# Kernel tuning notes

Measured on AMD Instinct MI355X. Metric: run time of the kernel, lower is better.

Reference implementation:

```python
import jax, jax.numpy as jnp
import numpy as np

B, N, T, L, H = 8, 128, 256, 32, 128


def setup_inputs() -> dict:
    key = jax.random.key(0)
    k0, k1, k2, k3, k4, k5 = jax.random.split(key, 6)
    x = jax.random.uniform(k0, (B, N, T), dtype=jnp.float32)
    s = 1.0 / np.sqrt(H)  # pytorch LSTM/Linear default init scale
    W_ih = jax.random.uniform(k1, (N, 4 * H, L), minval=-s, maxval=s, dtype=jnp.float32)
    b_ih = jax.random.uniform(k2, (N, 4 * H), minval=-s, maxval=s, dtype=jnp.float32)
    b_hh = jax.random.uniform(k3, (N, 4 * H), minval=-s, maxval=s, dtype=jnp.float32)
    W_fc = jax.random.uniform(k4, (N, N, H), minval=-s, maxval=s, dtype=jnp.float32)  # [node_i, out_j, H]
    b_fc = jax.random.uniform(k5, (N, N), minval=-s, maxval=s, dtype=jnp.float32)  # [node_i, out_j]
    return {"x": x, "W_ih": W_ih, "b_ih": b_ih, "b_hh": b_hh, "W_fc": W_fc, "b_fc": b_fc}


def reference(x, W_ih, b_ih, b_hh, W_fc, b_fc):
    # x: [B, N, T]
    Bn, Nn, Tn = x.shape
    Ln = W_ih.shape[-1]
    Hh = W_fc.shape[-1]
    Ttau = Tn - Ln  # number of prediction steps (t = L .. T-1)

    # Sliding windows x[:, i, tau:tau+L] for tau = 0..Ttau-1  -> [B, N, Ttau, L]
    idx = jnp.arange(Ttau)[:, None] + jnp.arange(Ln)[None, :]  # [Ttau, L]
    xw = x[:, :, idx]

    # Single-step LSTM with zero initial state: W_hh term vanishes.
    gates = jnp.einsum('bntl,ngl->bntg', xw, W_ih) + (b_ih + b_hh)[None, :, None, :]
    gi, gf, gg, go = jnp.split(gates, 4, axis=-1)  # pytorch order: i, f, g, o
    c = jax.nn.sigmoid(gi) * jnp.tanh(gg)          # f*c0 = 0
    h = jax.nn.sigmoid(go) * jnp.tanh(c)           # [B, N, Ttau, H]

    # Per-node fc (grouped GEMM): contributions[b, tau, j, i]
    contrib = jnp.einsum('bnth,njh->btjn', h, W_fc) + b_fc.T[None, None, :, :]

    # G[b, j, i] = mean_tau contrib[b, tau, j, i] / x[b, i, L + tau]
    denom = jnp.transpose(x[:, :, Ln:], (0, 2, 1))[:, :, None, :]  # [B, Ttau, 1, N_i]
    G = jnp.mean(contrib / denom, axis=1)                          # [B, N, N]

    X_hat = jnp.sum(contrib, axis=2) + 1e-6  # [B, Ttau, N]
    return G, X_hat
```

## Files before the change

kernel.cpp:

```cpp
#include <hip/hip_runtime.h>
#include <math.h>

#define B_  8
#define N_  128
#define T_  256
#define L_  32
#define H_  128
#define TT_ 224

typedef float f4    __attribute__((ext_vector_type(4)));
typedef float f32x4 __attribute__((ext_vector_type(4)));
typedef short bf16x8 __attribute__((ext_vector_type(8)));

__device__ __forceinline__ unsigned pk2bf(float a, float b) {
    unsigned ua = __float_as_uint(a), ub = __float_as_uint(b);
    ua = (ua + 0x7FFFu + ((ua >> 16) & 1u)) >> 16;
    ub = (ub + 0x7FFFu + ((ub >> 16) & 1u)) >> 16;
    return ua | (ub << 16);
}

__global__ __launch_bounds__(256)
void k_pre(const float* __restrict__ W_ih, const float* __restrict__ W_fc,
           const float* __restrict__ b_ih, const float* __restrict__ b_hh,
           const float* __restrict__ b_fc,
           unsigned short* __restrict__ W3sw, float* __restrict__ wsum,
           float* __restrict__ bsum, float* __restrict__ bia_g) {
    const int n   = blockIdx.x;
    const int pid = blockIdx.y;
    const int tid = threadIdx.x;
    if (pid < 6) {
        const int idx  = pid * 256 + tid;
        const int fg   = idx >> 6;
        const int lane = idx & 63;
        const int col  = lane & 15, quad = lane >> 4;
        const int g    = fg % 3, ht = fg / 3;
        const int r    = g * 128 + ht * 16 + col;
        const int sr   = r + (r >= 128 ? 128 : 0);
        const f4* src = (const f4*)(W_ih + (size_t)n * 512 * L_ + sr * L_ + quad * 8);
        f4 v0 = src[0], v1 = src[1];
        uint4 out;
        out.x = pk2bf(v0.x, v0.y); out.y = pk2bf(v0.z, v0.w);
        out.z = pk2bf(v1.x, v1.y); out.w = pk2bf(v1.z, v1.w);
        *(uint4*)&W3sw[((size_t)n * 1536 + idx) * 8] = out;
    } else {
        __shared__ f4 part[8][32];
        __shared__ float bp[2];
        {
            const int h4 = tid & 31, jg = tid >> 5;
            const f4* Wf = (const f4*)(W_fc + (size_t)n * N_ * H_) + (size_t)jg * 16 * 32 + h4;
            f4 s = {0.f, 0.f, 0.f, 0.f};
            #pragma unroll
            for (int j = 0; j < 16; ++j) s += Wf[j * 32];
            part[jg][h4] = s;
        }
        if (tid < 128) {
            float bv = b_fc[n * N_ + tid];
            #pragma unroll
            for (int off = 32; off > 0; off >>= 1) bv += __shfl_down(bv, off, 64);
            if ((tid & 63) == 0) bp[tid >> 6] = bv;
        }
        for (int i = tid; i < 384; i += 256) {
            const int sr = i + (i >= 128 ? 128 : 0);
            bia_g[n * 384 + i] = b_ih[(size_t)n * 512 + sr] + b_hh[(size_t)n * 512 + sr];
        }
        __syncthreads();
        if (tid < 32) {
            f4 s = part[0][tid];
            #pragma unroll
            for (int jg = 1; jg < 8; ++jg) s += part[jg][tid];
            *(f4*)&wsum[n * H_ + tid * 4] = s;
        }
        if (tid == 0) bsum[n] = bp[0] + bp[1];
    }
}

__global__ __launch_bounds__(256)
__attribute__((amdgpu_waves_per_eu(4, 4)))
void k_main(const float* __restrict__ x,
            const unsigned short* __restrict__ W3sw,
            const float* __restrict__ bia_g,
            const float* __restrict__ wsum, const float* __restrict__ bsum,
            const float* __restrict__ W_fc, const float* __restrict__ b_fc,
            float* __restrict__ G, float* __restrict__ xhat) {
    const int n   = blockIdx.x;
    const int b   = blockIdx.y;
    const int tid = threadIdx.x;
    const int w    = tid >> 6;
    const int lane = tid & 63;
    const int col  = lane & 15;
    const int quad = lane >> 4;

    __shared__ float xs[258];
    __shared__ unsigned xeo[2][128];
    __shared__ float xr[TT_];
    __shared__ uint4 xA[14 * 64];
    __shared__ float xh_part[4][TT_];
    __shared__ float hd_loc[H_];
    __shared__ float red[4];

    const uint4* wsw = (const uint4*)W3sw + (size_t)n * 24 * 64 + lane;
    union { uint4 u; bf16x8 v; } bfr[2][3];
    float biaL[2][3], wshL[2];
    #pragma unroll
    for (int ht2 = 0; ht2 < 2; ++ht2) {
        const int ht = 2 * w + ht2;
        #pragma unroll
        for (int g = 0; g < 3; ++g) {
            bfr[ht2][g].u = wsw[(size_t)(ht * 3 + g) * 64];
            biaL[ht2][g]  = bia_g[n * 384 + g * 128 + ht * 16 + col];
        }
        wshL[ht2] = wsum[n * H_ + ht * 16 + col];
    }
    const float bsum_n = bsum[n];

    xs[tid] = x[((size_t)b * N_ + n) * T_ + tid];
    if (tid < 2) xs[256 + tid] = 0.f;
    __syncthreads();
    if (tid < TT_) xr[tid] = 1.0f / xs[L_ + tid];
    if (tid < 128) {
        xeo[0][tid] = pk2bf(xs[2 * tid],     xs[2 * tid + 1]);
        xeo[1][tid] = pk2bf(xs[2 * tid + 1], xs[2 * tid + 2]);
    }
    __syncthreads();
    for (int e = tid; e < 14 * 64; e += 256) {
        const int tt = e >> 6, ln = e & 63;
        const int s  = tt * 16 + (ln & 15) + (ln >> 4) * 8;
        const int p  = s & 1, base = s >> 1;
        uint4 v;
        v.x = xeo[p][base + 0]; v.y = xeo[p][base + 1];
        v.z = xeo[p][base + 2]; v.w = xeo[p][base + 3];
        xA[e] = v;
    }
    __syncthreads();

    float hd_acc[2] = {0.f, 0.f};
    const f32x4 zero4 = {0.f, 0.f, 0.f, 0.f};

    #pragma unroll 2
    for (int ttile = 0; ttile < 14; ++ttile) {
        union { uint4 u; bf16x8 v; } af;
        af.u = xA[ttile * 64 + lane];

        const f4 xr4 = *(const f4*)&xr[ttile * 16 + quad * 4];
        float px[4] = {0.f, 0.f, 0.f, 0.f};

        #pragma unroll
        for (int ht2 = 0; ht2 < 2; ++ht2) {
            f32x4 ai = __builtin_amdgcn_mfma_f32_16x16x32_bf16(af.v, bfr[ht2][0].v, zero4, 0, 0, 0);
            f32x4 ag = __builtin_amdgcn_mfma_f32_16x16x32_bf16(af.v, bfr[ht2][1].v, zero4, 0, 0, 0);
            f32x4 ao = __builtin_amdgcn_mfma_f32_16x16x32_bf16(af.v, bfr[ht2][2].v, zero4, 0, 0, 0);
            #pragma unroll
            for (int reg = 0; reg < 4; ++reg) {
                const float gi = ai[reg] + biaL[ht2][0];
                const float gg = ag[reg] + biaL[ht2][1];
                const float go = ao[reg] + biaL[ht2][2];
                const float e1 = __expf(-gi);
                const float e2 = __expf(gg + gg);
                const float c  = (e2 - 1.f) *
                    __builtin_amdgcn_rcpf((1.f + e1) * (e2 + 1.f));
                const float e3 = __expf(-go);
                const float e4 = __expf(c + c);
                const float hh = (e4 - 1.f) *
                    __builtin_amdgcn_rcpf((1.f + e3) * (e4 + 1.f));
                hd_acc[ht2] = fmaf(hh, xr4[reg], hd_acc[ht2]);
                px[reg]     = fmaf(hh, wshL[ht2], px[reg]);
            }
        }
        #pragma unroll
        for (int reg = 0; reg < 4; ++reg) {
            float pv = px[reg];
            pv += __shfl_xor(pv, 1, 64);
            pv += __shfl_xor(pv, 2, 64);
            pv += __shfl_xor(pv, 4, 64);
            pv += __shfl_xor(pv, 8, 64);
            if (col == 0) xh_part[w][ttile * 16 + quad * 4 + reg] = pv;
        }
    }

    #pragma unroll
    for (int ht2 = 0; ht2 < 2; ++ht2) {
        float v = hd_acc[ht2];
        v += __shfl_xor(v, 16, 64);
        v += __shfl_xor(v, 32, 64);
        if (lane < 16) hd_loc[(2 * w + ht2) * 16 + lane] = v;
    }
    {
        float dv = (tid < TT_) ? xr[tid] : 0.f;
        #pragma unroll
        for (int off = 32; off > 0; off >>= 1) dv += __shfl_down(dv, off, 64);
        if (lane == 0) red[w] = dv;
    }
    __syncthreads();

    if (tid < TT_) {
        const float v = xh_part[0][tid] + xh_part[1][tid] +
                        xh_part[2][tid] + xh_part[3][tid];
        xhat[((size_t)b * TT_ + tid) * N_ + n] = v + bsum_n + 1e-6f;
    }

    {
        const float dinv = red[0] + red[1] + red[2] + red[3];
        const int j    = tid >> 1;
        const int half = tid & 1;
        const f4* Wf = (const f4*)(W_fc + ((size_t)n * N_ + j) * H_ + half * 64);
        float s = 0.f;
        #pragma unroll
        for (int q = 0; q < 16; ++q) {
            const f4 wv = Wf[q];
            const int hb = half * 64 + q * 4;
            s = fmaf(wv.x, hd_loc[hb + 0],
                fmaf(wv.y, hd_loc[hb + 1],
                fmaf(wv.z, hd_loc[hb + 2],
                fmaf(wv.w, hd_loc[hb + 3], s))));
        }
        s += __shfl_xor(s, 1, 64);
        if (half == 0) {
            const float bj = b_fc[n * N_ + j];
            G[(size_t)b * N_ * N_ + (size_t)j * N_ + n] =
                (s + bj * dinv) * (1.0f / 224.0f);
        }
    }
}

extern "C" void kernel_launch(void* const* d_in, const int* in_sizes, int n_in,
                              void* d_out, int out_size, void* d_ws, size_t ws_size,
                              hipStream_t stream) {
    const float* x    = (const float*)d_in[0];
    const float* W_ih = (const float*)d_in[1];
    const float* b_ih = (const float*)d_in[2];
    const float* b_hh = (const float*)d_in[3];
    const float* W_fc = (const float*)d_in[4];
    const float* b_fc = (const float*)d_in[5];

    float* G    = (float*)d_out;
    float* xhat = (float*)d_out + (size_t)B_ * N_ * N_;

    unsigned short* W3sw = (unsigned short*)d_ws;
    float* wsum  = (float*)(W3sw + (size_t)N_ * 1536 * 8);
    float* bsum  = wsum + N_ * H_;
    float* bia_g = bsum + N_;

    k_pre<<<dim3(N_, 7), dim3(256), 0, stream>>>(W_ih, W_fc, b_ih, b_hh, b_fc,
                                                 W3sw, wsum, bsum, bia_g);
    k_main<<<dim3(N_, B_), dim3(256), 0, stream>>>(x, W3sw, bia_g, wsum, bsum,
                                                   W_fc, b_fc, G, xhat);
}
```

Measured before the change: 114.5 us.

## Split time axis across blocks, move G projection to separate kernel, fold log2e into weights

```diff
diff --git a/kernel.cpp b/kernel.cpp
--- a/kernel.cpp
+++ b/kernel.cpp
@@ -12,11 +12,20 @@
 typedef float f32x4 __attribute__((ext_vector_type(4)));
 typedef short bf16x8 __attribute__((ext_vector_type(8)));
 
+#define L2E_  1.4426950408889634f
+#define L2E2_ 2.8853900817779268f
+
 __device__ __forceinline__ unsigned pk2bf(float a, float b) {
     unsigned ua = __float_as_uint(a), ub = __float_as_uint(b);
     ua = (ua + 0x7FFFu + ((ua >> 16) & 1u)) >> 16;
     ub = (ub + 0x7FFFu + ((ub >> 16) & 1u)) >> 16;
     return ua | (ub << 16);
+}
+__device__ __forceinline__ float aexp2(float x) {
+    float r; asm("v_exp_f32 %0, %1" : "=v"(r) : "v"(x)); return r;
+}
+__device__ __forceinline__ float aexp2n(float x) {
+    float r; asm("v_exp_f32 %0, -%1" : "=v"(r) : "v"(x)); return r;
 }
 
 __global__ __launch_bounds__(256)
@@ -36,8 +45,9 @@
         const int g    = fg % 3, ht = fg / 3;
         const int r    = g * 128 + ht * 16 + col;
         const int sr   = r + (r >= 128 ? 128 : 0);
+        const float sc = (g == 1) ? L2E2_ : L2E_;
         const f4* src = (const f4*)(W_ih + (size_t)n * 512 * L_ + sr * L_ + quad * 8);
-        f4 v0 = src[0], v1 = src[1];
+        f4 v0 = src[0] * sc, v1 = src[1] * sc;
         uint4 out;
         out.x = pk2bf(v0.x, v0.y); out.y = pk2bf(v0.z, v0.w);
         out.z = pk2bf(v1.x, v1.y); out.w = pk2bf(v1.z, v1.w);
@@ -61,7 +71,9 @@
         }
         for (int i = tid; i < 384; i += 256) {
             const int sr = i + (i >= 128 ? 128 : 0);
-            bia_g[n * 384 + i] = b_ih[(size_t)n * 512 + sr] + b_hh[(size_t)n * 512 + sr];
+            const float sc = (i >= 128 && i < 256) ? L2E2_ : L2E_;
+            bia_g[n * 384 + i] =
+                (b_ih[(size_t)n * 512 + sr] + b_hh[(size_t)n * 512 + sr]) * sc;
         }
         __syncthreads();
         if (tid < 32) {
@@ -75,16 +87,17 @@
 }
 
 __global__ __launch_bounds__(256)
-__attribute__((amdgpu_waves_per_eu(4, 4)))
+__attribute__((amdgpu_waves_per_eu(8)))
 void k_main(const float* __restrict__ x,
             const unsigned short* __restrict__ W3sw,
             const float* __restrict__ bia_g,
             const float* __restrict__ wsum, const float* __restrict__ bsum,
-            const float* __restrict__ W_fc, const float* __restrict__ b_fc,
-            float* __restrict__ G, float* __restrict__ xhat) {
-    const int n   = blockIdx.x;
-    const int b   = blockIdx.y;
-    const int tid = threadIdx.x;
+            float* __restrict__ Hd_part, float* __restrict__ Dinv_part,
+            float* __restrict__ xhat) {
+    const int n    = blockIdx.x;
+    const int b    = blockIdx.y;
+    const int half = blockIdx.z;
+    const int tid  = threadIdx.x;
     const int w    = tid >> 6;
     const int lane = tid & 63;
     const int col  = lane & 15;
@@ -92,10 +105,9 @@
 
     __shared__ float xs[258];
     __shared__ unsigned xeo[2][128];
-    __shared__ float xr[TT_];
-    __shared__ uint4 xA[14 * 64];
-    __shared__ float xh_part[4][TT_];
-    __shared__ float hd_loc[H_];
+    __shared__ float xr_loc[112];
+    __shared__ uint4 xA[7 * 64];
+    __shared__ float xh_part[4][112];
     __shared__ float red[4];
 
     const uint4* wsw = (const uint4*)W3sw + (size_t)n * 24 * 64 + lane;
@@ -116,15 +128,15 @@
     xs[tid] = x[((size_t)b * N_ + n) * T_ + tid];
     if (tid < 2) xs[256 + tid] = 0.f;
     __syncthreads();
-    if (tid < TT_) xr[tid] = 1.0f / xs[L_ + tid];
+    if (tid < 112) xr_loc[tid] = 1.0f / xs[L_ + half * 112 + tid];
     if (tid < 128) {
         xeo[0][tid] = pk2bf(xs[2 * tid],     xs[2 * tid + 1]);
         xeo[1][tid] = pk2bf(xs[2 * tid + 1], xs[2 * tid + 2]);
     }
     __syncthreads();
-    for (int e = tid; e < 14 * 64; e += 256) {
+    for (int e = tid; e < 7 * 64; e += 256) {
         const int tt = e >> 6, ln = e & 63;
-        const int s  = tt * 16 + (ln & 15) + (ln >> 4) * 8;
+        const int s  = (half * 7 + tt) * 16 + (ln & 15) + (ln >> 4) * 8;
         const int p  = s & 1, base = s >> 1;
         uint4 v;
         v.x = xeo[p][base + 0]; v.y = xeo[p][base + 1];
@@ -137,11 +149,11 @@
     const f32x4 zero4 = {0.f, 0.f, 0.f, 0.f};
 
     #pragma unroll 2
-    for (int ttile = 0; ttile < 14; ++ttile) {
+    for (int tt = 0; tt < 7; ++tt) {
         union { uint4 u; bf16x8 v; } af;
-        af.u = xA[ttile * 64 + lane];
-
-        const f4 xr4 = *(const f4*)&xr[ttile * 16 + quad * 4];
+        af.u = xA[tt * 64 + lane];
+
+        const f4 xr4 = *(const f4*)&xr_loc[tt * 16 + quad * 4];
         float px[4] = {0.f, 0.f, 0.f, 0.f};
 
         #pragma unroll
@@ -154,12 +166,12 @@
                 const float gi = ai[reg] + biaL[ht2][0];
                 const float gg = ag[reg] + biaL[ht2][1];
                 const float go = ao[reg] + biaL[ht2][2];
-                const float e1 = __expf(-gi);
-                const float e2 = __expf(gg + gg);
+                const float e1 = aexp2n(gi);
+                const float e2 = aexp2(gg);
                 const float c  = (e2 - 1.f) *
                     __builtin_amdgcn_rcpf((1.f + e1) * (e2 + 1.f));
-                const float e3 = __expf(-go);
-                const float e4 = __expf(c + c);
+                const float e3 = aexp2n(go);
+                const float e4 = aexp2(c * L2E2_);
                 const float hh = (e4 - 1.f) *
                     __builtin_amdgcn_rcpf((1.f + e3) * (e4 + 1.f));
                 hd_acc[ht2] = fmaf(hh, xr4[reg], hd_acc[ht2]);
@@ -173,7 +185,7 @@
             pv += __shfl_xor(pv, 2, 64);
             pv += __shfl_xor(pv, 4, 64);
             pv += __shfl_xor(pv, 8, 64);
-            if (col == 0) xh_part[w][ttile * 16 + quad * 4 + reg] = pv;
+            if (col == 0) xh_part[w][tt * 16 + quad * 4 + reg] = pv;
         }
     }
 
@@ -182,43 +194,84 @@
         float v = hd_acc[ht2];
         v += __shfl_xor(v, 16, 64);
         v += __shfl_xor(v, 32, 64);
-        if (lane < 16) hd_loc[(2 * w + ht2) * 16 + lane] = v;
+        if (lane < 16)
+            Hd_part[(((size_t)half * B_ + b) * N_ + n) * H_ + (2 * w + ht2) * 16 + lane] = v;
     }
     {
-        float dv = (tid < TT_) ? xr[tid] : 0.f;
+        float dv = (tid < 112) ? xr_loc[tid] : 0.f;
         #pragma unroll
         for (int off = 32; off > 0; off >>= 1) dv += __shfl_down(dv, off, 64);
         if (lane == 0) red[w] = dv;
     }
     __syncthreads();
-
-    if (tid < TT_) {
+    if (tid == 0)
+        Dinv_part[((size_t)half * B_ + b) * N_ + n] = red[0] + red[1] + red[2] + red[3];
+
+    if (tid < 112) {
         const float v = xh_part[0][tid] + xh_part[1][tid] +
                         xh_part[2][tid] + xh_part[3][tid];
-        xhat[((size_t)b * TT_ + tid) * N_ + n] = v + bsum_n + 1e-6f;
-    }
-
-    {
-        const float dinv = red[0] + red[1] + red[2] + red[3];
-        const int j    = tid >> 1;
-        const int half = tid & 1;
-        const f4* Wf = (const f4*)(W_fc + ((size_t)n * N_ + j) * H_ + half * 64);
+        xhat[((size_t)b * TT_ + half * 112 + tid) * N_ + n] = v + bsum_n + 1e-6f;
+    }
+}
+
+__global__ __launch_bounds__(256)
+void k_g(const float* __restrict__ W_fc, const float* __restrict__ b_fc,
+         const float* __restrict__ Hd_part, const float* __restrict__ Dinv_part,
+         float* __restrict__ G) {
+    const int n  = blockIdx.x;
+    const int j0 = blockIdx.y * 16;
+    const int tid = threadIdx.x;
+
+    __shared__ float ws[16][132];
+    __shared__ float hd_s[B_][132];
+    __shared__ float dinv_s[B_];
+    __shared__ float pacc[16][16][8];
+
+    const f4* Wg = (const f4*)(W_fc + ((size_t)n * N_ + j0) * H_);
+    #pragma unroll
+    for (int k = 0; k < 2; ++k) {
+        const int i = tid + k * 256;
+        *(f4*)&ws[i >> 5][(i & 31) * 4] = Wg[i];
+    }
+    for (int i = tid; i < B_ * H_; i += 256) {
+        const int bb = i >> 7, hh = i & 127;
+        hd_s[bb][hh] = Hd_part[((size_t)bb * N_ + n) * H_ + hh] +
+                       Hd_part[(((size_t)B_ + bb) * N_ + n) * H_ + hh];
+    }
+    if (tid < B_)
+        dinv_s[tid] = Dinv_part[(size_t)tid * N_ + n] +
+                      Dinv_part[((size_t)B_ + tid) * N_ + n];
+    __syncthreads();
+
+    const int jl = tid >> 4;
+    const int cl = tid & 15;
+    float acc[B_];
+    #pragma unroll
+    for (int bb = 0; bb < B_; ++bb) acc[bb] = 0.f;
+    #pragma unroll
+    for (int q = 0; q < 2; ++q) {
+        const f4 wv = *(const f4*)&ws[jl][cl * 8 + q * 4];
+        const int hb = cl * 8 + q * 4;
+        #pragma unroll
+        for (int bb = 0; bb < B_; ++bb) {
+            acc[bb] = fmaf(wv.x, hd_s[bb][hb + 0],
+                      fmaf(wv.y, hd_s[bb][hb + 1],
+                      fmaf(wv.z, hd_s[bb][hb + 2],
+                      fmaf(wv.w, hd_s[bb][hb + 3], acc[bb]))));
+        }
+    }
+    #pragma unroll
+    for (int bb = 0; bb < B_; ++bb) pacc[jl][cl][bb] = acc[bb];
+    __syncthreads();
+
+    if (tid < 128) {
+        const int j2 = tid >> 3, bb = tid & 7;
         float s = 0.f;
         #pragma unroll
-        for (int q = 0; q < 16; ++q) {
-            const f4 wv = Wf[q];
-            const int hb = half * 64 + q * 4;
-            s = fmaf(wv.x, hd_loc[hb + 0],
-                fmaf(wv.y, hd_loc[hb + 1],
-                fmaf(wv.z, hd_loc[hb + 2],
-                fmaf(wv.w, hd_loc[hb + 3], s))));
-        }
-        s += __shfl_xor(s, 1, 64);
-        if (half == 0) {
-            const float bj = b_fc[n * N_ + j];
-            G[(size_t)b * N_ * N_ + (size_t)j * N_ + n] =
-                (s + bj * dinv) * (1.0f / 224.0f);
-        }
+        for (int c = 0; c < 16; ++c) s += pacc[j2][c][bb];
+        const float bj = b_fc[n * N_ + j0 + j2];
+        G[(size_t)bb * N_ * N_ + (size_t)(j0 + j2) * N_ + n] =
+            (s + bj * dinv_s[bb]) * (1.0f / 224.0f);
     }
 }
 
@@ -236,12 +289,15 @@
     float* xhat = (float*)d_out + (size_t)B_ * N_ * N_;
 
     unsigned short* W3sw = (unsigned short*)d_ws;
-    float* wsum  = (float*)(W3sw + (size_t)N_ * 1536 * 8);
-    float* bsum  = wsum + N_ * H_;
-    float* bia_g = bsum + N_;
+    float* wsum   = (float*)(W3sw + (size_t)N_ * 1536 * 8);
+    float* bsum   = wsum + N_ * H_;
+    float* bia_g  = bsum + N_;
+    float* Hd_p   = bia_g + N_ * 384;
+    float* Dinv_p = Hd_p + (size_t)2 * B_ * N_ * H_;
 
     k_pre<<<dim3(N_, 7), dim3(256), 0, stream>>>(W_ih, W_fc, b_ih, b_hh, b_fc,
                                                  W3sw, wsum, bsum, bia_g);
-    k_main<<<dim3(N_, B_), dim3(256), 0, stream>>>(x, W3sw, bia_g, wsum, bsum,
-                                                   W_fc, b_fc, G, xhat);
-}
+    k_main<<<dim3(N_, B_, 2), dim3(256), 0, stream>>>(x, W3sw, bia_g, wsum, bsum,
+                                                      Hd_p, Dinv_p, xhat);
+    k_g<<<dim3(N_, 8), dim3(256), 0, stream>>>(W_fc, b_fc, Hd_p, Dinv_p, G);
+}
```

Measured after the change: 158.8 us. +38.8%, slower.
